# Kernel optimization log

Hardware: AMD Instinct MI355X
Metric: run time of the kernel (lower is better)

Reference implementation:

```python
import jax, jax.numpy as jnp
import numpy as np

N_NODES = 100000
N_EDGES = 3200000


def spmm(row, col, val, x):
    # out[i] = sum_{e: row[e]==i} val[e] * x[col[e]]  -- sparse adj @ x
    return jax.ops.segment_sum(val[:, None] * x[col], row, num_segments=N_NODES)


def setup_inputs() -> dict:
    key = jax.random.key(0)
    k1, k2, k3, k4, k5, k6 = jax.random.split(key, 6)
    out_feat, hid_feat, in_feat = 32, 64, 128
    # xavier_uniform bounds
    b1 = float(np.sqrt(6.0 / (out_feat + hid_feat)))
    b2 = float(np.sqrt(6.0 / (hid_feat + in_feat)))
    return {
        "feat": jax.random.normal(k1, (N_NODES, out_feat), dtype=jnp.float32),
        "W1": jax.random.uniform(k2, (out_feat, hid_feat), minval=-b1, maxval=b1, dtype=jnp.float32),
        "W2": jax.random.uniform(k3, (hid_feat, in_feat), minval=-b2, maxval=b2, dtype=jnp.float32),
        "edge_row": jax.random.randint(k4, (N_EDGES,), 0, N_NODES, dtype=jnp.int32),
        "edge_col": jax.random.randint(k5, (N_EDGES,), 0, N_NODES, dtype=jnp.int32),
        "edge_val": jax.random.uniform(k6, (N_EDGES,), dtype=jnp.float32),
    }


def reference(feat, W1, W2, edge_row, edge_col, edge_val):
    x = feat @ W1                                  # [N, hid]
    x = spmm(edge_row, edge_col, edge_val, x)      # adj @ x
    # add_act=False: no activation
    x = x @ W2                                     # [N, in_feat]
    x = spmm(edge_row, edge_col, edge_val, x)      # adj @ x
    return x
```

## Files before the change

### kernel.cpp

```cpp
#include <hip/hip_runtime.h>

#define N_NODES 100000
#define N_EDGES 3200000
#define RPB 128
#define NB ((N_NODES + RPB - 1) / RPB)

typedef unsigned short ushort_t;
typedef unsigned int uint_t;

__device__ __forceinline__ ushort_t f32_to_bf16_rne(float f) {
    uint_t b = __float_as_uint(f);
    return (ushort_t)((b + 0x7FFFu + ((b >> 16) & 1u)) >> 16);
}
__device__ __forceinline__ float bf16_to_f32(ushort_t u) {
    return __uint_as_float(((uint_t)u) << 16);
}


__global__ void gemm_w12_kernel(const float* __restrict__ W1,
                                const float* __restrict__ W2,
                                float* __restrict__ W12) {
    int idx = blockIdx.x * blockDim.x + threadIdx.x;
    if (idx >= 32 * 128) return;
    int r = idx >> 7;
    int c = idx & 127;
    float acc = 0.f;
#pragma unroll
    for (int k = 0; k < 64; ++k) acc += W1[r * 64 + k] * W2[k * 128 + c];
    W12[idx] = acc;
}

__global__ void cvt_bf16_kernel(const float* __restrict__ in, ushort_t* __restrict__ ob) {
    int i = blockIdx.x * blockDim.x + threadIdx.x;
    if (i < N_NODES * 32) ob[i] = f32_to_bf16_rne(in[i]);
}

__global__ void gemm_out_kernel(const float* __restrict__ g2,
                                const float* __restrict__ W12,
                                float* __restrict__ out) {
    int tid = threadIdx.x;
    int jo = (tid & 31) * 4;
    int rl = tid >> 5;
    float4 w[32];
#pragma unroll
    for (int k = 0; k < 32; ++k) w[k] = *(const float4*)&W12[k * 128 + jo];
    for (int r = blockIdx.x * 8 + rl; r < N_NODES; r += gridDim.x * 8) {
        const float4* g4 = (const float4*)(g2 + (size_t)r * 32);
        float4 acc = make_float4(0.f, 0.f, 0.f, 0.f);
#pragma unroll
        for (int q = 0; q < 8; ++q) {
            float4 gv = g4[q];
            int k = q * 4;
            acc.x += gv.x * w[k].x;     acc.y += gv.x * w[k].y;
            acc.z += gv.x * w[k].z;     acc.w += gv.x * w[k].w;
            acc.x += gv.y * w[k + 1].x; acc.y += gv.y * w[k + 1].y;
            acc.z += gv.y * w[k + 1].z; acc.w += gv.y * w[k + 1].w;
            acc.x += gv.z * w[k + 2].x; acc.y += gv.z * w[k + 2].y;
            acc.z += gv.z * w[k + 2].z; acc.w += gv.z * w[k + 2].w;
            acc.x += gv.w * w[k + 3].x; acc.y += gv.w * w[k + 3].y;
            acc.z += gv.w * w[k + 3].z; acc.w += gv.w * w[k + 3].w;
        }
        *(float4*)&out[(size_t)r * 128 + jo] = acc;
    }
}


__global__ void hist_bucket_kernel(const int* __restrict__ row, int* __restrict__ cnt) {
    __shared__ int h[NB];
    for (int t = threadIdx.x; t < NB; t += blockDim.x) h[t] = 0;
    __syncthreads();
    int per = (N_EDGES + gridDim.x - 1) / gridDim.x;
    int s = blockIdx.x * per;
    int e = min(s + per, N_EDGES);
    for (int i = s + threadIdx.x; i < e; i += blockDim.x)
        atomicAdd(&h[row[i] >> 7], 1);
    __syncthreads();
    for (int t = threadIdx.x; t < NB; t += blockDim.x)
        if (h[t]) atomicAdd(&cnt[t], h[t]);
}

__global__ void scan_bucket_kernel(const int* __restrict__ cnt,
                                   int* __restrict__ offs, int* __restrict__ cur_b) {
    __shared__ int s[1024];
    int t = threadIdx.x;
    int v = (t < NB) ? cnt[t] : 0;
    s[t] = v;
    __syncthreads();
    for (int off = 1; off < 1024; off <<= 1) {
        int add = (t >= off) ? s[t - off] : 0;
        __syncthreads();
        s[t] += add;
        __syncthreads();
    }
    if (t < NB) { int x = s[t] - v; offs[t] = x; cur_b[t] = x; }
    if (t == 0) offs[NB] = N_EDGES;
}

__global__ void scatter_bucket_kernel(const int* __restrict__ row, const int* __restrict__ col,
                                      const float* __restrict__ val,
                                      int* __restrict__ cur_b, int2* __restrict__ ebuf) {
    __shared__ int h[NB];
    __shared__ int base[NB];
    for (int t = threadIdx.x; t < NB; t += blockDim.x) h[t] = 0;
    __syncthreads();
    int per = (N_EDGES + gridDim.x - 1) / gridDim.x;
    int s = blockIdx.x * per;
    int e = min(s + per, N_EDGES);
    for (int i = s + threadIdx.x; i < e; i += blockDim.x)
        atomicAdd(&h[row[i] >> 7], 1);
    __syncthreads();
    for (int t = threadIdx.x; t < NB; t += blockDim.x) {
        int c = h[t];
        base[t] = c ? atomicAdd(&cur_b[t], c) : 0;
        h[t] = 0;
    }
    __syncthreads();
    for (int i = s + threadIdx.x; i < e; i += blockDim.x) {
        int r = row[i];
        int b = r >> 7;
        int lp = atomicAdd(&h[b], 1);
        ebuf[base[b] + lp] = make_int2((col[i] << 7) | (r & 127), __float_as_int(val[i]));
    }
}

__global__ void rowsort_kernel(const int* __restrict__ offs, const int2* __restrict__ ebuf,
                               int2* __restrict__ ep, int* __restrict__ rs) {
    __shared__ int h[RPB];
    __shared__ int loff[RPB];
    __shared__ int curl[RPB];
    int b = blockIdx.x;
    int s = offs[b], e = offs[b + 1];
    int t = threadIdx.x;
    if (t < RPB) h[t] = 0;
    __syncthreads();
    for (int i = s + t; i < e; i += blockDim.x)
        atomicAdd(&h[ebuf[i].x & 127], 1);
    __syncthreads();
    if (t < RPB) loff[t] = h[t];
    __syncthreads();
    for (int off = 1; off < RPB; off <<= 1) {
        int add = (t < RPB && t >= off) ? loff[t - off] : 0;
        __syncthreads();
        if (t < RPB) loff[t] += add;
        __syncthreads();
    }
    if (t < RPB) {
        int excl = loff[t] - h[t];
        curl[t] = excl;
        int r = b * RPB + t;
        if (r < N_NODES) rs[r] = s + excl;
    }
    if (b == 0 && t == 0) rs[N_NODES] = N_EDGES;
    __syncthreads();
    for (int i = s + t; i < e; i += blockDim.x) {
        int2 cv = ebuf[i];
        int rl = cv.x & 127;
        int pos = s + atomicAdd(&curl[rl], 1);
        ep[pos] = make_int2(cv.x >> 7, cv.y);
    }
}

template <bool OUT_BF16>
__global__ void spmm_csr_kernel(const int* __restrict__ rs,
                                const int2* __restrict__ ep,
                                const ushort_t* __restrict__ xb,
                                void* __restrict__ outv) {
    int gid = blockIdx.x * blockDim.x + threadIdx.x;
    int r = gid >> 6;
    if (r >= N_NODES) return;
    int lane = threadIdx.x & 63;
    int j = lane & 31;
    int half = lane >> 5;
    int s = rs[r], e = rs[r + 1];
    float a0 = 0.f, a1 = 0.f, a2 = 0.f, a3 = 0.f;
    int p = s + half;
    for (; p + 14 < e; p += 16) {
        int2 c0 = ep[p];
        int2 c1 = ep[p + 2];
        int2 c2 = ep[p + 4];
        int2 c3 = ep[p + 6];
        int2 c4 = ep[p + 8];
        int2 c5 = ep[p + 10];
        int2 c6 = ep[p + 12];
        int2 c7 = ep[p + 14];
        ushort_t u0 = xb[c0.x * 32 + j];
        ushort_t u1 = xb[c1.x * 32 + j];
        ushort_t u2 = xb[c2.x * 32 + j];
        ushort_t u3 = xb[c3.x * 32 + j];
        ushort_t u4 = xb[c4.x * 32 + j];
        ushort_t u5 = xb[c5.x * 32 + j];
        ushort_t u6 = xb[c6.x * 32 + j];
        ushort_t u7 = xb[c7.x * 32 + j];
        a0 += __int_as_float(c0.y) * bf16_to_f32(u0);
        a1 += __int_as_float(c1.y) * bf16_to_f32(u1);
        a2 += __int_as_float(c2.y) * bf16_to_f32(u2);
        a3 += __int_as_float(c3.y) * bf16_to_f32(u3);
        a0 += __int_as_float(c4.y) * bf16_to_f32(u4);
        a1 += __int_as_float(c5.y) * bf16_to_f32(u5);
        a2 += __int_as_float(c6.y) * bf16_to_f32(u6);
        a3 += __int_as_float(c7.y) * bf16_to_f32(u7);
    }
    for (; p + 6 < e; p += 8) {
        int2 c0 = ep[p];
        int2 c1 = ep[p + 2];
        int2 c2 = ep[p + 4];
        int2 c3 = ep[p + 6];
        ushort_t u0 = xb[c0.x * 32 + j];
        ushort_t u1 = xb[c1.x * 32 + j];
        ushort_t u2 = xb[c2.x * 32 + j];
        ushort_t u3 = xb[c3.x * 32 + j];
        a0 += __int_as_float(c0.y) * bf16_to_f32(u0);
        a1 += __int_as_float(c1.y) * bf16_to_f32(u1);
        a2 += __int_as_float(c2.y) * bf16_to_f32(u2);
        a3 += __int_as_float(c3.y) * bf16_to_f32(u3);
    }
    for (; p < e; p += 2) {
        int2 cv = ep[p];
        a0 += __int_as_float(cv.y) * bf16_to_f32(xb[cv.x * 32 + j]);
    }
    float acc = (a0 + a1) + (a2 + a3);
    acc += __shfl_xor(acc, 32, 64);
    if (half == 0) {
        if constexpr (OUT_BF16) {
            ((ushort_t*)outv)[r * 32 + j] = f32_to_bf16_rne(acc);
        } else {
            ((float*)outv)[r * 32 + j] = acc;
        }
    }
}

__global__ void spmm32_atomic_kernel(const int* __restrict__ row,
                                     const int* __restrict__ col,
                                     const float* __restrict__ val,
                                     const float* __restrict__ x,
                                     float* __restrict__ out) {
    int id = blockIdx.x * blockDim.x + threadIdx.x;
    int e = id >> 5;
    int j = id & 31;
    if (e >= N_EDGES) return;
    atomicAdd(&out[row[e] * 32 + j], val[e] * x[col[e] * 32 + j]);
}

__global__ void gemm_out_fallback_kernel(const float* __restrict__ g2,
                                         const float* __restrict__ W12,
                                         float* __restrict__ out) {
    int id = blockIdx.x * blockDim.x + threadIdx.x;
    int i = id >> 7;
    int j = id & 127;
    const float* g = g2 + i * 32;
    float acc = 0.f;
#pragma unroll
    for (int k = 0; k < 32; ++k) acc += g[k] * W12[k * 128 + j];
    out[id] = acc;
}

extern "C" void kernel_launch(void* const* d_in, const int* in_sizes, int n_in,
                              void* d_out, int out_size, void* d_ws, size_t ws_size,
                              hipStream_t stream) {
    const float* feat = (const float*)d_in[0];
    const float* W1   = (const float*)d_in[1];
    const float* W2   = (const float*)d_in[2];
    const int*   erow = (const int*)d_in[3];
    const int*   ecol = (const int*)d_in[4];
    const float* eval_= (const float*)d_in[5];
    float* out = (float*)d_out;

    float*    W12   = (float*)d_ws;
    ushort_t* xb    = (ushort_t*)(W12 + 4096);
    ushort_t* g1b   = xb + (size_t)N_NODES * 32;
    float*    g2    = (float*)(g1b + (size_t)N_NODES * 32);
    int2*     ep    = (int2*)(g2 + (size_t)N_NODES * 32);
    int*      cnt   = (int*)(ep + N_EDGES);
    int*      offs  = cnt + NB;
    int*      cur_b = offs + NB + 1;
    int*      rs    = cur_b + NB;
    size_t    needed = (size_t)((char*)(rs + N_NODES + 2) - (char*)d_ws);

    int2* ebuf = (int2*)d_out;

    gemm_w12_kernel<<<16, 256, 0, stream>>>(W1, W2, W12);

    if (ws_size >= needed) {
        cvt_bf16_kernel<<<(N_NODES * 32 + 255) / 256, 256, 0, stream>>>(feat, xb);

        hipMemsetAsync(cnt, 0, NB * sizeof(int), stream);
        hist_bucket_kernel<<<256, 1024, 0, stream>>>(erow, cnt);
        scan_bucket_kernel<<<1, 1024, 0, stream>>>(cnt, offs, cur_b);
        scatter_bucket_kernel<<<256, 1024, 0, stream>>>(erow, ecol, eval_, cur_b, ebuf);
        rowsort_kernel<<<NB, 512, 0, stream>>>(offs, ebuf, ep, rs);

        spmm_csr_kernel<true><<<(N_NODES * 64) / 256, 256, 0, stream>>>(rs, ep, xb, g1b);
        spmm_csr_kernel<false><<<(N_NODES * 64) / 256, 256, 0, stream>>>(rs, ep, g1b, g2);

        gemm_out_kernel<<<1024, 256, 0, stream>>>(g2, W12, out);
    } else {
        float* g1f = (float*)d_ws + 4096;
        float* g2f = g1f + (size_t)N_NODES * 32;
        hipMemsetAsync(g1f, 0, (size_t)N_NODES * 32 * 2 * sizeof(float), stream);
        spmm32_atomic_kernel<<<(N_EDGES * 32) / 256, 256, 0, stream>>>(erow, ecol, eval_, feat, g1f);
        spmm32_atomic_kernel<<<(N_EDGES * 32) / 256, 256, 0, stream>>>(erow, ecol, eval_, g1f, g2f);
        gemm_out_fallback_kernel<<<(N_NODES * 128) / 256, 256, 0, stream>>>(g2f, W12, out);
    }
}
```

Measured before the change: 284.5 us.

## Split feature columns into two 16-wide halves for cache-resident SpMM gathers

The 32-wide bf16 feature matrix is stored as two separate 16-column halves, and each SpMM runs twice, once per half, so the gathered table (3.2 MB per half) is more likely to stay in L2 during random column gathers. The CSR edge stream is read with nontemporal 64-bit loads, and outputs are written with nontemporal stores. Each wave now processes four edges in parallel with 16 lanes each. The cost is reading the edge list twice per SpMM stage and launching two more kernels.

```diff
diff --git a/kernel.cpp b/kernel.cpp
--- a/kernel.cpp
+++ b/kernel.cpp
@@ -30,12 +30,19 @@
     W12[idx] = acc;
 }
 
-__global__ void cvt_bf16_kernel(const float* __restrict__ in, ushort_t* __restrict__ ob) {
+__global__ void cvt_split_kernel(const float* __restrict__ in,
+                                 ushort_t* __restrict__ lo, ushort_t* __restrict__ hi) {
     int i = blockIdx.x * blockDim.x + threadIdx.x;
-    if (i < N_NODES * 32) ob[i] = f32_to_bf16_rne(in[i]);
-}
-
-__global__ void gemm_out_kernel(const float* __restrict__ g2,
+    if (i >= N_NODES * 32) return;
+    int r = i >> 5;
+    int j = i & 31;
+    ushort_t v = f32_to_bf16_rne(in[i]);
+    if (j < 16) lo[r * 16 + j] = v;
+    else        hi[r * 16 + (j - 16)] = v;
+}
+
+__global__ void gemm_out_kernel(const float* __restrict__ g2lo,
+                                const float* __restrict__ g2hi,
                                 const float* __restrict__ W12,
                                 float* __restrict__ out) {
     int tid = threadIdx.x;
@@ -45,11 +52,12 @@
 #pragma unroll
     for (int k = 0; k < 32; ++k) w[k] = *(const float4*)&W12[k * 128 + jo];
     for (int r = blockIdx.x * 8 + rl; r < N_NODES; r += gridDim.x * 8) {
-        const float4* g4 = (const float4*)(g2 + (size_t)r * 32);
+        const float4* glo = (const float4*)(g2lo + (size_t)r * 16);
+        const float4* ghi = (const float4*)(g2hi + (size_t)r * 16);
         float4 acc = make_float4(0.f, 0.f, 0.f, 0.f);
 #pragma unroll
         for (int q = 0; q < 8; ++q) {
-            float4 gv = g4[q];
+            float4 gv = (q < 4) ? glo[q] : ghi[q - 4];
             int k = q * 4;
             acc.x += gv.x * w[k].x;     acc.y += gv.x * w[k].y;
             acc.z += gv.x * w[k].z;     acc.w += gv.x * w[k].w;
@@ -161,70 +169,50 @@
 }
 
 template <bool OUT_BF16>
-__global__ void spmm_csr_kernel(const int* __restrict__ rs,
-                                const int2* __restrict__ ep,
-                                const ushort_t* __restrict__ xb,
-                                void* __restrict__ outv) {
+__global__ void spmm_half_kernel(const int* __restrict__ rs,
+                                 const long long* __restrict__ ep,
+                                 const ushort_t* __restrict__ xb,
+                                 void* __restrict__ outv) {
     int gid = blockIdx.x * blockDim.x + threadIdx.x;
     int r = gid >> 6;
     if (r >= N_NODES) return;
     int lane = threadIdx.x & 63;
-    int j = lane & 31;
-    int half = lane >> 5;
+    int j = lane & 15;
+    int g = lane >> 4;
     int s = rs[r], e = rs[r + 1];
-    float a0 = 0.f, a1 = 0.f, a2 = 0.f, a3 = 0.f;
-    int p = s + half;
-    for (; p + 14 < e; p += 16) {
-        int2 c0 = ep[p];
-        int2 c1 = ep[p + 2];
-        int2 c2 = ep[p + 4];
-        int2 c3 = ep[p + 6];
-        int2 c4 = ep[p + 8];
-        int2 c5 = ep[p + 10];
-        int2 c6 = ep[p + 12];
-        int2 c7 = ep[p + 14];
-        ushort_t u0 = xb[c0.x * 32 + j];
-        ushort_t u1 = xb[c1.x * 32 + j];
-        ushort_t u2 = xb[c2.x * 32 + j];
-        ushort_t u3 = xb[c3.x * 32 + j];
-        ushort_t u4 = xb[c4.x * 32 + j];
-        ushort_t u5 = xb[c5.x * 32 + j];
-        ushort_t u6 = xb[c6.x * 32 + j];
-        ushort_t u7 = xb[c7.x * 32 + j];
-        a0 += __int_as_float(c0.y) * bf16_to_f32(u0);
-        a1 += __int_as_float(c1.y) * bf16_to_f32(u1);
-        a2 += __int_as_float(c2.y) * bf16_to_f32(u2);
-        a3 += __int_as_float(c3.y) * bf16_to_f32(u3);
-        a0 += __int_as_float(c4.y) * bf16_to_f32(u4);
-        a1 += __int_as_float(c5.y) * bf16_to_f32(u5);
-        a2 += __int_as_float(c6.y) * bf16_to_f32(u6);
-        a3 += __int_as_float(c7.y) * bf16_to_f32(u7);
-    }
-    for (; p + 6 < e; p += 8) {
-        int2 c0 = ep[p];
-        int2 c1 = ep[p + 2];
-        int2 c2 = ep[p + 4];
-        int2 c3 = ep[p + 6];
-        ushort_t u0 = xb[c0.x * 32 + j];
-        ushort_t u1 = xb[c1.x * 32 + j];
-        ushort_t u2 = xb[c2.x * 32 + j];
-        ushort_t u3 = xb[c3.x * 32 + j];
-        a0 += __int_as_float(c0.y) * bf16_to_f32(u0);
-        a1 += __int_as_float(c1.y) * bf16_to_f32(u1);
-        a2 += __int_as_float(c2.y) * bf16_to_f32(u2);
-        a3 += __int_as_float(c3.y) * bf16_to_f32(u3);
-    }
-    for (; p < e; p += 2) {
-        int2 cv = ep[p];
-        a0 += __int_as_float(cv.y) * bf16_to_f32(xb[cv.x * 32 + j]);
-    }
-    float acc = (a0 + a1) + (a2 + a3);
+    float a0 = 0.f, a1 = 0.f;
+    int p = s + g;
+    for (; p + 12 < e; p += 16) {
+        long long v0 = __builtin_nontemporal_load(ep + p);
+        long long v1 = __builtin_nontemporal_load(ep + p + 4);
+        long long v2 = __builtin_nontemporal_load(ep + p + 8);
+        long long v3 = __builtin_nontemporal_load(ep + p + 12);
+        int c0 = (int)(v0 & 0xffffffffLL), w0 = (int)(v0 >> 32);
+        int c1 = (int)(v1 & 0xffffffffLL), w1 = (int)(v1 >> 32);
+        int c2 = (int)(v2 & 0xffffffffLL), w2 = (int)(v2 >> 32);
+        int c3 = (int)(v3 & 0xffffffffLL), w3 = (int)(v3 >> 32);
+        ushort_t u0 = xb[c0 * 16 + j];
+        ushort_t u1 = xb[c1 * 16 + j];
+        ushort_t u2 = xb[c2 * 16 + j];
+        ushort_t u3 = xb[c3 * 16 + j];
+        a0 += __int_as_float(w0) * bf16_to_f32(u0);
+        a1 += __int_as_float(w1) * bf16_to_f32(u1);
+        a0 += __int_as_float(w2) * bf16_to_f32(u2);
+        a1 += __int_as_float(w3) * bf16_to_f32(u3);
+    }
+    for (; p < e; p += 4) {
+        long long v = __builtin_nontemporal_load(ep + p);
+        int c = (int)(v & 0xffffffffLL), w = (int)(v >> 32);
+        a0 += __int_as_float(w) * bf16_to_f32(xb[c * 16 + j]);
+    }
+    float acc = a0 + a1;
+    acc += __shfl_xor(acc, 16, 64);
     acc += __shfl_xor(acc, 32, 64);
-    if (half == 0) {
+    if (g == 0) {
         if constexpr (OUT_BF16) {
-            ((ushort_t*)outv)[r * 32 + j] = f32_to_bf16_rne(acc);
+            __builtin_nontemporal_store(f32_to_bf16_rne(acc), (ushort_t*)outv + r * 16 + j);
         } else {
-            ((float*)outv)[r * 32 + j] = acc;
+            __builtin_nontemporal_store(acc, (float*)outv + r * 16 + j);
         }
     }
 }
@@ -266,10 +254,13 @@
     float* out = (float*)d_out;
 
     float*    W12   = (float*)d_ws;
-    ushort_t* xb    = (ushort_t*)(W12 + 4096);
-    ushort_t* g1b   = xb + (size_t)N_NODES * 32;
-    float*    g2    = (float*)(g1b + (size_t)N_NODES * 32);
-    int2*     ep    = (int2*)(g2 + (size_t)N_NODES * 32);
+    ushort_t* xb_lo = (ushort_t*)(W12 + 4096);
+    ushort_t* xb_hi = xb_lo + (size_t)N_NODES * 16;
+    ushort_t* g1_lo = xb_hi + (size_t)N_NODES * 16;
+    ushort_t* g1_hi = g1_lo + (size_t)N_NODES * 16;
+    float*    g2_lo = (float*)(g1_hi + (size_t)N_NODES * 16);
+    float*    g2_hi = g2_lo + (size_t)N_NODES * 16;
+    int2*     ep    = (int2*)(g2_hi + (size_t)N_NODES * 16);
     int*      cnt   = (int*)(ep + N_EDGES);
     int*      offs  = cnt + NB;
     int*      cur_b = offs + NB + 1;
@@ -281,7 +272,7 @@
     gemm_w12_kernel<<<16, 256, 0, stream>>>(W1, W2, W12);
 
     if (ws_size >= needed) {
-        cvt_bf16_kernel<<<(N_NODES * 32 + 255) / 256, 256, 0, stream>>>(feat, xb);
+        cvt_split_kernel<<<(N_NODES * 32 + 255) / 256, 256, 0, stream>>>(feat, xb_lo, xb_hi);
 
         hipMemsetAsync(cnt, 0, NB * sizeof(int), stream);
         hist_bucket_kernel<<<256, 1024, 0, stream>>>(erow, cnt);
@@ -289,10 +280,14 @@
         scatter_bucket_kernel<<<256, 1024, 0, stream>>>(erow, ecol, eval_, cur_b, ebuf);
         rowsort_kernel<<<NB, 512, 0, stream>>>(offs, ebuf, ep, rs);
 
-        spmm_csr_kernel<true><<<(N_NODES * 64) / 256, 256, 0, stream>>>(rs, ep, xb, g1b);
-        spmm_csr_kernel<false><<<(N_NODES * 64) / 256, 256, 0, stream>>>(rs, ep, g1b, g2);
-
-        gemm_out_kernel<<<1024, 256, 0, stream>>>(g2, W12, out);
+        const long long* epl = (const long long*)ep;
+        int spmm_grid = (N_NODES * 64) / 256;
+        spmm_half_kernel<true><<<spmm_grid, 256, 0, stream>>>(rs, epl, xb_lo, g1_lo);
+        spmm_half_kernel<true><<<spmm_grid, 256, 0, stream>>>(rs, epl, xb_hi, g1_hi);
+        spmm_half_kernel<false><<<spmm_grid, 256, 0, stream>>>(rs, epl, g1_lo, g2_lo);
+        spmm_half_kernel<false><<<spmm_grid, 256, 0, stream>>>(rs, epl, g1_hi, g2_hi);
+
+        gemm_out_kernel<<<1024, 256, 0, stream>>>(g2_lo, g2_hi, W12, out);
     } else {
         float* g1f = (float*)d_ws + 4096;
         float* g2f = g1f + (size_t)N_NODES * 32;
```

New measurement: 417.6 us. +46.8%, slower.

## Gather packed bf16 pairs with four edge groups per wave in grid-stride SpMM

Applied to the files above, without the earlier changes.

The CSR SpMM kernel now has each lane load a 32-bit word holding two bf16 features, so 16 lanes cover a 32-wide row and a wave processes four edges at a time instead of two. Partial sums are reduced with two xor shuffles and written as packed pairs. The launch becomes a fixed 2048-block grid-stride loop over rows instead of one wave per row. This is meant to widen memory transactions and increase edge-level parallelism, at the cost of more shuffles and a possible load imbalance from the fixed grid.

```diff
diff --git a/kernel.cpp b/kernel.cpp
--- a/kernel.cpp
+++ b/kernel.cpp
@@ -12,8 +12,11 @@
     uint_t b = __float_as_uint(f);
     return (ushort_t)((b + 0x7FFFu + ((b >> 16) & 1u)) >> 16);
 }
-__device__ __forceinline__ float bf16_to_f32(ushort_t u) {
-    return __uint_as_float(((uint_t)u) << 16);
+__device__ __forceinline__ float bf16_lo(uint_t u) {
+    return __uint_as_float(u << 16);
+}
+__device__ __forceinline__ float bf16_hi(uint_t u) {
+    return __uint_as_float(u & 0xffff0000u);
 }
 
 
@@ -163,68 +166,72 @@
 template <bool OUT_BF16>
 __global__ void spmm_csr_kernel(const int* __restrict__ rs,
                                 const int2* __restrict__ ep,
-                                const ushort_t* __restrict__ xb,
+                                const uint_t* __restrict__ xb,
                                 void* __restrict__ outv) {
     int gid = blockIdx.x * blockDim.x + threadIdx.x;
-    int r = gid >> 6;
-    if (r >= N_NODES) return;
+    int wid = gid >> 6;
+    int nwaves = (gridDim.x * blockDim.x) >> 6;
     int lane = threadIdx.x & 63;
-    int j = lane & 31;
-    int half = lane >> 5;
-    int s = rs[r], e = rs[r + 1];
-    float a0 = 0.f, a1 = 0.f, a2 = 0.f, a3 = 0.f;
-    int p = s + half;
-    for (; p + 14 < e; p += 16) {
-        int2 c0 = ep[p];
-        int2 c1 = ep[p + 2];
-        int2 c2 = ep[p + 4];
-        int2 c3 = ep[p + 6];
-        int2 c4 = ep[p + 8];
-        int2 c5 = ep[p + 10];
-        int2 c6 = ep[p + 12];
-        int2 c7 = ep[p + 14];
-        ushort_t u0 = xb[c0.x * 32 + j];
-        ushort_t u1 = xb[c1.x * 32 + j];
-        ushort_t u2 = xb[c2.x * 32 + j];
-        ushort_t u3 = xb[c3.x * 32 + j];
-        ushort_t u4 = xb[c4.x * 32 + j];
-        ushort_t u5 = xb[c5.x * 32 + j];
-        ushort_t u6 = xb[c6.x * 32 + j];
-        ushort_t u7 = xb[c7.x * 32 + j];
-        a0 += __int_as_float(c0.y) * bf16_to_f32(u0);
-        a1 += __int_as_float(c1.y) * bf16_to_f32(u1);
-        a2 += __int_as_float(c2.y) * bf16_to_f32(u2);
-        a3 += __int_as_float(c3.y) * bf16_to_f32(u3);
-        a0 += __int_as_float(c4.y) * bf16_to_f32(u4);
-        a1 += __int_as_float(c5.y) * bf16_to_f32(u5);
-        a2 += __int_as_float(c6.y) * bf16_to_f32(u6);
-        a3 += __int_as_float(c7.y) * bf16_to_f32(u7);
-    }
-    for (; p + 6 < e; p += 8) {
-        int2 c0 = ep[p];
-        int2 c1 = ep[p + 2];
-        int2 c2 = ep[p + 4];
-        int2 c3 = ep[p + 6];
-        ushort_t u0 = xb[c0.x * 32 + j];
-        ushort_t u1 = xb[c1.x * 32 + j];
-        ushort_t u2 = xb[c2.x * 32 + j];
-        ushort_t u3 = xb[c3.x * 32 + j];
-        a0 += __int_as_float(c0.y) * bf16_to_f32(u0);
-        a1 += __int_as_float(c1.y) * bf16_to_f32(u1);
-        a2 += __int_as_float(c2.y) * bf16_to_f32(u2);
-        a3 += __int_as_float(c3.y) * bf16_to_f32(u3);
-    }
-    for (; p < e; p += 2) {
-        int2 cv = ep[p];
-        a0 += __int_as_float(cv.y) * bf16_to_f32(xb[cv.x * 32 + j]);
-    }
-    float acc = (a0 + a1) + (a2 + a3);
-    acc += __shfl_xor(acc, 32, 64);
-    if (half == 0) {
-        if constexpr (OUT_BF16) {
-            ((ushort_t*)outv)[r * 32 + j] = f32_to_bf16_rne(acc);
-        } else {
-            ((float*)outv)[r * 32 + j] = acc;
+    int j2 = lane & 15;
+    int g = lane >> 4;
+    for (int r = wid; r < N_NODES; r += nwaves) {
+        int s = rs[r], e = rs[r + 1];
+        float a0 = 0.f, a1 = 0.f, b0 = 0.f, b1 = 0.f;
+        int p = s + g;
+        for (; p + 28 < e; p += 32) {
+            int2 c0 = ep[p];
+            int2 c1 = ep[p + 4];
+            int2 c2 = ep[p + 8];
+            int2 c3 = ep[p + 12];
+            int2 c4 = ep[p + 16];
+            int2 c5 = ep[p + 20];
+            int2 c6 = ep[p + 24];
+            int2 c7 = ep[p + 28];
+            uint_t u0 = xb[c0.x * 16 + j2];
+            uint_t u1 = xb[c1.x * 16 + j2];
+            uint_t u2 = xb[c2.x * 16 + j2];
+            uint_t u3 = xb[c3.x * 16 + j2];
+            uint_t u4 = xb[c4.x * 16 + j2];
+            uint_t u5 = xb[c5.x * 16 + j2];
+            uint_t u6 = xb[c6.x * 16 + j2];
+            uint_t u7 = xb[c7.x * 16 + j2];
+            float w0 = __int_as_float(c0.y);
+            float w1 = __int_as_float(c1.y);
+            float w2 = __int_as_float(c2.y);
+            float w3 = __int_as_float(c3.y);
+            float w4 = __int_as_float(c4.y);
+            float w5 = __int_as_float(c5.y);
+            float w6 = __int_as_float(c6.y);
+            float w7 = __int_as_float(c7.y);
+            a0 += w0 * bf16_lo(u0); a1 += w0 * bf16_hi(u0);
+            b0 += w1 * bf16_lo(u1); b1 += w1 * bf16_hi(u1);
+            a0 += w2 * bf16_lo(u2); a1 += w2 * bf16_hi(u2);
+            b0 += w3 * bf16_lo(u3); b1 += w3 * bf16_hi(u3);
+            a0 += w4 * bf16_lo(u4); a1 += w4 * bf16_hi(u4);
+            b0 += w5 * bf16_lo(u5); b1 += w5 * bf16_hi(u5);
+            a0 += w6 * bf16_lo(u6); a1 += w6 * bf16_hi(u6);
+            b0 += w7 * bf16_lo(u7); b1 += w7 * bf16_hi(u7);
+        }
+        for (; p < e; p += 4) {
+            int2 cv = ep[p];
+            uint_t u = xb[cv.x * 16 + j2];
+            float w = __int_as_float(cv.y);
+            a0 += w * bf16_lo(u);
+            a1 += w * bf16_hi(u);
+        }
+        float r0 = a0 + b0;
+        float r1 = a1 + b1;
+        r0 += __shfl_xor(r0, 16, 64);
+        r0 += __shfl_xor(r0, 32, 64);
+        r1 += __shfl_xor(r1, 16, 64);
+        r1 += __shfl_xor(r1, 32, 64);
+        if (g == 0) {
+            if constexpr (OUT_BF16) {
+                uint_t pk = (uint_t)f32_to_bf16_rne(r0) | ((uint_t)f32_to_bf16_rne(r1) << 16);
+                ((uint_t*)outv)[r * 16 + j2] = pk;
+            } else {
+                ((float2*)outv)[r * 16 + j2] = make_float2(r0, r1);
+            }
         }
     }
 }
@@ -289,8 +296,8 @@
         scatter_bucket_kernel<<<256, 1024, 0, stream>>>(erow, ecol, eval_, cur_b, ebuf);
         rowsort_kernel<<<NB, 512, 0, stream>>>(offs, ebuf, ep, rs);
 
-        spmm_csr_kernel<true><<<(N_NODES * 64) / 256, 256, 0, stream>>>(rs, ep, xb, g1b);
-        spmm_csr_kernel<false><<<(N_NODES * 64) / 256, 256, 0, stream>>>(rs, ep, g1b, g2);
+        spmm_csr_kernel<true><<<2048, 256, 0, stream>>>(rs, ep, (const uint_t*)xb, g1b);
+        spmm_csr_kernel<false><<<2048, 256, 0, stream>>>(rs, ep, (const uint_t*)g1b, g2);
 
         gemm_out_kernel<<<1024, 256, 0, stream>>>(g2, W12, out);
     } else {
```

New measurement: 269.8 us. -5.1%, faster.
